# Optimization experiments

Measured on AMD Instinct MI355X. Metric: run time of the kernel, lower is better.

The kernel has to match this reference:

```python
import math
import jax, jax.numpy as jnp
import numpy as np

B, LQ, LK, D, DV = 16, 2048, 2048, 256, 256


def setup_inputs() -> dict:
    key = jax.random.key(0)
    k1, k2, k3, k4 = jax.random.split(key, 4)
    query = jax.random.normal(k1, (B, LQ, D), dtype=jnp.float32)
    kmat = jax.random.normal(k2, (B, LK, D), dtype=jnp.float32)
    value = jax.random.normal(k3, (B, LK, DV), dtype=jnp.float32)
    # per-batch valid lengths in [1, LK] (avoid 0 => all -inf row)
    valid_len = jax.random.randint(k4, (B,), 1, LK + 1, dtype=jnp.int64)
    return {"query": query, "key": kmat, "value": value, "valid_len": valid_len}


def reference(query, key, value, valid_len):
    d = query.shape[-1]
    # [B, Lq, Lk] scaled dot-product scores
    scores = jnp.einsum("bqd,bkd->bqk", query, key) / math.sqrt(d)
    # mask positions k >= valid_len[b] (same mask broadcast over all queries,
    # matching the repeat(1, Lq).view(shape) in the original masked_softmax)
    mask = jnp.arange(key.shape[1])[None, None, :] < valid_len[:, None, None]
    scores = jnp.where(mask, scores, -jnp.inf)
    attn = jax.nn.softmax(scores, axis=-1)  # dropout rate is 0.0 => identity
    return jnp.einsum("bqk,bkv->bqv", attn, value)
```

## Files before the change

### kernel.cpp

```cpp
#include <hip/hip_runtime.h>
#include <hip/hip_bf16.h>

#define B_   16
#define LQ_  2048
#define LK_  2048
#define D_   256
#define DV_  256
#define MINF -1.0e30f

typedef __bf16 bf16x8_t __attribute__((ext_vector_type(8)));
typedef short  s16x8    __attribute__((ext_vector_type(8)));
typedef short  s16x4    __attribute__((ext_vector_type(4)));
typedef float  f32x4    __attribute__((ext_vector_type(4)));

__device__ __forceinline__ unsigned short f2bf(float f) {
  unsigned int u = __builtin_bit_cast(unsigned int, f);
  u += 0x7fffu + ((u >> 16) & 1u);
  return (unsigned short)(u >> 16);
}

__device__ __forceinline__ s16x8 pack8(float4 a, float4 b) {
  s16x8 r;
  r[0] = (short)f2bf(a.x); r[1] = (short)f2bf(a.y);
  r[2] = (short)f2bf(a.z); r[3] = (short)f2bf(a.w);
  r[4] = (short)f2bf(b.x); r[5] = (short)f2bf(b.y);
  r[6] = (short)f2bf(b.z); r[7] = (short)f2bf(b.w);
  return r;
}

__device__ __forceinline__ void glds16(const unsigned short* g, unsigned short* l) {
  __builtin_amdgcn_global_load_lds(
      (const __attribute__((address_space(1))) unsigned int*)g,
      (__attribute__((address_space(3))) unsigned int*)l, 16, 0, 0);
}

__global__ __launch_bounds__(256) void prep_k(const float* __restrict__ K,
                                              unsigned short* __restrict__ wsK) {
  int gid = blockIdx.x * 256 + threadIdx.x;
  int gr = gid >> 5;
  int c  = gid & 31;
  const float* src = K + ((size_t)gr << 8) + c * 8;
  float4 a = *(const float4*)(src);
  float4 b = *(const float4*)(src + 4);
  *(s16x8*)(wsK + ((size_t)gr << 8) + ((c ^ (gr & 7)) << 3)) = pack8(a, b);
}

__global__ __launch_bounds__(256) void prep_v(const float* __restrict__ V,
                                              unsigned short* __restrict__ wsV) {
  __shared__ unsigned short t[256 * 72];
  const int tid = threadIdx.x;
  const float* src = V + (size_t)blockIdx.x * 64 * 256;
  #pragma unroll
  for (int i = 0; i < 16; ++i) {
    int idx = i * 256 + tid;
    int k   = idx >> 6;
    int dv0 = (idx & 63) * 4;
    float4 x = *(const float4*)(src + k * 256 + dv0);
    t[(dv0 + 0) * 72 + k] = f2bf(x.x);
    t[(dv0 + 1) * 72 + k] = f2bf(x.y);
    t[(dv0 + 2) * 72 + k] = f2bf(x.z);
    t[(dv0 + 3) * 72 + k] = f2bf(x.w);
  }
  __syncthreads();
  unsigned short* dst = wsV + (size_t)blockIdx.x * 16384;
  #pragma unroll
  for (int i = 0; i < 8; ++i) {
    int idx = i * 256 + tid;
    int dv = idx >> 3;
    int ch = idx & 7;
    s16x8 v = *(const s16x8*)(&t[dv * 72 + ch * 8]);
    *(s16x8*)(dst + dv * 64 + ((ch ^ (dv & 7)) << 3)) = v;
  }
}

__global__ __launch_bounds__(256) void prep_sched(const int* __restrict__ VL,
                                                  int* __restrict__ sched) {
  __shared__ int ord[16];
  if (threadIdx.x == 0) {
    int nk[16], o[16];
    const int wide = (VL[1] == 0);
    for (int i = 0; i < 16; ++i) {
      int v = wide ? VL[2 * i] : VL[i];
      if (v < 1) v = 1;
      if (v > LK_) v = LK_;
      nk[i] = v; o[i] = i;
    }
    for (int i = 1; i < 16; ++i) {
      int key = o[i], kv = nk[key], j = i - 1;
      while (j >= 0 && nk[o[j]] < kv) { o[j + 1] = o[j]; --j; }
      o[j + 1] = key;
    }
    for (int i = 0; i < 16; ++i) ord[i] = o[i];
  }
  __syncthreads();
  for (int s = threadIdx.x; s < 512; s += 256) {
    int w  = s & 255;
    int un = s >> 8;
    int i  = un ? (511 - w) : w;
    int bsel = ord[i >> 5];
    int qt   = i & 31;
    sched[s] = bsel | (qt << 8);
  }
}

__global__ __launch_bounds__(256, 1) void attn_fwd10(
    const float* __restrict__ Q, const unsigned short* __restrict__ wsK,
    const unsigned short* __restrict__ wsV, const int* __restrict__ VL,
    const int* __restrict__ sched, float* __restrict__ O) {
  __shared__ __align__(16) unsigned short lds_all[70144];

  const int tid  = threadIdx.x;
  const int wid  = tid >> 6;
  const int lane = tid & 63;
  const int l15  = lane & 15;
  const int lg   = lane >> 4;
  const int rq   = wid & 1;
  const int kh   = wid >> 1;

  unsigned short* pw = &lds_all[65536 + wid * 1152];

#define STAGE(buf, t) do {                                                    \
    const unsigned short* ks_ = kbw + (size_t)(t) * 16384;                    \
    const unsigned short* vs_ = vbw + (size_t)(t) * 16384;                    \
    _Pragma("unroll")                                                         \
    for (int p = 0; p < 8; ++p) {                                             \
      int cu = p * 256 + wid * 64;                                            \
      glds16(ks_ + (size_t)(cu + lane) * 8, &lds_all[(buf) * 16384 + cu * 8]);\
      glds16(vs_ + (size_t)(cu + lane) * 8,                                   \
             &lds_all[32768 + (buf) * 16384 + cu * 8]);                       \
    }                                                                         \
  } while (0)

  for (int un = 0; un < 2; ++un) {
    const int e  = sched[blockIdx.x + un * 256];
    const int b  = e & 255;
    const int qt = e >> 8;

    int n_k = (VL[1] == 0) ? VL[2 * b] : VL[b];
    if (n_k < 1) n_k = 1;
    if (n_k > LK_) n_k = LK_;
    const int nt = (n_k + 63) >> 6;

    const int qbase = qt * 64 + rq * 32;

    s16x8 qf[2][8];
    #pragma unroll
    for (int qc = 0; qc < 2; ++qc) {
      const float* qp = Q + ((size_t)b * LQ_ + qbase + qc * 16 + l15) * D_ + lg * 8;
      #pragma unroll
      for (int dk = 0; dk < 8; ++dk) {
        float4 a = *(const float4*)(qp + dk * 32);
        float4 c = *(const float4*)(qp + dk * 32 + 4);
        qf[qc][dk] = pack8(a, c);
      }
    }

    f32x4 o[2][16];
    #pragma unroll
    for (int qc = 0; qc < 2; ++qc)
      #pragma unroll
      for (int c = 0; c < 16; ++c) o[qc][c] = (f32x4){0.f, 0.f, 0.f, 0.f};
    float m[2] = {MINF, MINF}, l[2] = {0.f, 0.f};

    const unsigned short* kbw = wsK + (size_t)b * LK_ * D_;
    const unsigned short* vbw = wsV + (size_t)b * LK_ * DV_;

    __syncthreads();
    STAGE(0, 0);

    for (int t = 0; t < nt; ++t) {
      const int cur = t & 1;
      if (t + 1 < nt) {
        STAGE(cur ^ 1, t + 1);
        asm volatile("s_waitcnt vmcnt(16)" ::: "memory");
      } else {
        asm volatile("s_waitcnt vmcnt(0)" ::: "memory");
      }
      __builtin_amdgcn_s_barrier();
      __builtin_amdgcn_sched_barrier(0);

      const unsigned short* kl = &lds_all[cur * 16384];
      f32x4 s[2][2];
      __builtin_amdgcn_s_setprio(1);
      #pragma unroll
      for (int kc = 0; kc < 2; ++kc) {
        int krow = kh * 32 + kc * 16 + l15;
        int sw = (krow & 7) << 3;
        const unsigned short* kbase = kl + krow * 256;
        f32x4 a0 = (f32x4){0.f, 0.f, 0.f, 0.f};
        f32x4 a1 = (f32x4){0.f, 0.f, 0.f, 0.f};
        #pragma unroll
        for (int dk = 0; dk < 8; ++dk) {
          s16x8 kf = *(const s16x8*)(kbase + ((dk * 32 + lg * 8) ^ sw));
          a0 = __builtin_amdgcn_mfma_f32_16x16x32_bf16(
              __builtin_bit_cast(bf16x8_t, kf),
              __builtin_bit_cast(bf16x8_t, qf[0][dk]), a0, 0, 0, 0);
          a1 = __builtin_amdgcn_mfma_f32_16x16x32_bf16(
              __builtin_bit_cast(bf16x8_t, kf),
              __builtin_bit_cast(bf16x8_t, qf[1][dk]), a1, 0, 0, 0);
        }
        s[kc][0] = a0;
        s[kc][1] = a1;
      }
      __builtin_amdgcn_s_setprio(0);

      #pragma unroll
      for (int kc = 0; kc < 2; ++kc) {
        int gk = t * 64 + kh * 32 + kc * 16 + lg * 4;
        #pragma unroll
        for (int qc = 0; qc < 2; ++qc)
          #pragma unroll
          for (int j2 = 0; j2 < 4; ++j2)
            s[kc][qc][j2] = (gk + j2 < n_k) ? s[kc][qc][j2] * 0.0625f : MINF;
      }

      float pml[2];
      #pragma unroll
      for (int qc = 0; qc < 2; ++qc) {
        float v = fmaxf(fmaxf(s[0][qc][0], s[0][qc][1]),
                        fmaxf(s[0][qc][2], s[0][qc][3]));
        v = fmaxf(v, fmaxf(fmaxf(s[1][qc][0], s[1][qc][1]),
                           fmaxf(s[1][qc][2], s[1][qc][3])));
        pml[qc] = v;
      }
      if (__any((pml[0] > m[0] + 8.0f) || (pml[1] > m[1] + 8.0f))) {
        #pragma unroll
        for (int qc = 0; qc < 2; ++qc) {
          float pm = fmaxf(pml[qc], __shfl_xor(pml[qc], 16, 64));
          pm = fmaxf(pm, __shfl_xor(pm, 32, 64));
          float mn = fmaxf(m[qc], pm);
          float sc = __expf(m[qc] - mn);
          m[qc] = mn; l[qc] *= sc;
          #pragma unroll
          for (int c = 0; c < 16; ++c) o[qc][c] = o[qc][c] * sc;
        }
      }
      #pragma unroll
      for (int qc = 0; qc < 2; ++qc) {
        float p[2][4];
        #pragma unroll
        for (int kc = 0; kc < 2; ++kc)
          #pragma unroll
          for (int j2 = 0; j2 < 4; ++j2)
            p[kc][j2] = __expf(s[kc][qc][j2] - m[qc]);
        l[qc] += ((p[0][0] + p[0][1]) + (p[0][2] + p[0][3]))
               + ((p[1][0] + p[1][1]) + (p[1][2] + p[1][3]));
        #pragma unroll
        for (int kc = 0; kc < 2; ++kc) {
          s16x4 w;
          w[0] = (short)f2bf(p[kc][0]); w[1] = (short)f2bf(p[kc][1]);
          w[2] = (short)f2bf(p[kc][2]); w[3] = (short)f2bf(p[kc][3]);
          *(s16x4*)(pw + (qc * 16 + l15) * 36 + kc * 16 + lg * 4) = w;
        }
      }

      s16x8 pb[2];
      #pragma unroll
      for (int qc = 0; qc < 2; ++qc)
        pb[qc] = *(const s16x8*)(pw + (qc * 16 + l15) * 36 + lg * 8);

      const unsigned short* vl_ = &lds_all[32768 + cur * 16384];
      __builtin_amdgcn_s_setprio(1);
      #pragma unroll
      for (int c = 0; c < 16; ++c) {
        int dv = c * 16 + l15;
        s16x8 vf = *(const s16x8*)(vl_ + dv * 64 + (((kh * 4 + lg) ^ (dv & 7)) << 3));
        o[0][c] = __builtin_amdgcn_mfma_f32_16x16x32_bf16(
            __builtin_bit_cast(bf16x8_t, vf),
            __builtin_bit_cast(bf16x8_t, pb[0]), o[0][c], 0, 0, 0);
        o[1][c] = __builtin_amdgcn_mfma_f32_16x16x32_bf16(
            __builtin_bit_cast(bf16x8_t, vf),
            __builtin_bit_cast(bf16x8_t, pb[1]), o[1][c], 0, 0, 0);
      }
      __builtin_amdgcn_s_setprio(0);

      __builtin_amdgcn_sched_barrier(0);
      __builtin_amdgcn_s_barrier();
    }

    #pragma unroll
    for (int qc = 0; qc < 2; ++qc) {
      l[qc] += __shfl_xor(l[qc], 16, 64);
      l[qc] += __shfl_xor(l[qc], 32, 64);
    }

    __syncthreads();
    float* mo = (float*)lds_all + rq * 8448;
    if (kh == 1) {
      #pragma unroll
      for (int qc = 0; qc < 2; ++qc) {
        #pragma unroll
        for (int c = 0; c < 16; ++c)
          *(f32x4*)(mo + (qc * 16 + l15) * 260 + c * 16 + lg * 4) = o[qc][c];
        mo[8320 + qc * 16 + l15] = m[qc];
        mo[8352 + qc * 16 + l15] = l[qc];
      }
    }
    __syncthreads();
    if (kh == 0) {
      #pragma unroll
      for (int qc = 0; qc < 2; ++qc) {
        float mb = mo[8320 + qc * 16 + l15];
        float lb = mo[8352 + qc * 16 + l15];
        float M  = fmaxf(m[qc], mb);
        float sa = __expf(m[qc] - M), sb = __expf(mb - M);
        float invL = 1.0f / (sa * l[qc] + sb * lb);
        float* ob = O + ((size_t)b * LQ_ + qbase + qc * 16 + l15) * DV_;
        #pragma unroll
        for (int c = 0; c < 16; ++c) {
          int dvb = c * 16 + lg * 4;
          f32x4 mr = *(const f32x4*)(mo + (qc * 16 + l15) * 260 + dvb);
          f32x4 r;
          #pragma unroll
          for (int j2 = 0; j2 < 4; ++j2)
            r[j2] = (sa * o[qc][c][j2] + sb * mr[j2]) * invL;
          *(f32x4*)(ob + dvb) = r;
        }
      }
    }
  }
#undef STAGE
}

__global__ __launch_bounds__(256) void attn_fwd(
    const float* __restrict__ Q, const float* __restrict__ K,
    const float* __restrict__ V, const int* __restrict__ VL,
    float* __restrict__ O) {
  __shared__ __align__(16) unsigned short lds_k[64 * D_];
  __shared__ __align__(16) unsigned short lds_v[DV_ * 64];
  __shared__ __align__(16) unsigned short lds_p[4][16 * 64];

  const int tid  = threadIdx.x;
  const int wid  = tid >> 6;
  const int lane = tid & 63;
  const int l15  = lane & 15;
  const int lg   = lane >> 4;
  const int bid = blockIdx.x;
  const int b   = bid >> 5;
  const int qt  = bid & 31;

  int n_k = (VL[1] == 0) ? VL[2 * b] : VL[b];
  if (n_k < 1) n_k = 1;
  if (n_k > LK_) n_k = LK_;

  const int qbase = qt * 64 + wid * 16;
  s16x8 qf[8];
  {
    const float* qp = Q + ((size_t)b * LQ_ + qbase + l15) * D_ + lg * 8;
    #pragma unroll
    for (int dk = 0; dk < 8; ++dk) {
      float4 a = *(const float4*)(qp + dk * 32);
      float4 c = *(const float4*)(qp + dk * 32 + 4);
      qf[dk] = pack8(a, c);
    }
  }
  f32x4 o[16];
  #pragma unroll
  for (int c = 0; c < 16; ++c) o[c] = (f32x4){0.f, 0.f, 0.f, 0.f};
  float m[4]    = {-INFINITY, -INFINITY, -INFINITY, -INFINITY};
  float lsum[4] = {0.f, 0.f, 0.f, 0.f};
  const float* kb = K + (size_t)b * LK_ * D_;
  const float* vb = V + (size_t)b * LK_ * DV_;
  const int nt = (n_k + 63) / 64;

  for (int kt = 0; kt < nt; ++kt) {
    __syncthreads();
    {
      const float* src = kb + (size_t)kt * 64 * D_;
      #pragma unroll
      for (int p = 0; p < 8; ++p) {
        int e = (p * 256 + tid) * 8;
        int r = e >> 8;
        int d = e & 255;
        float4 a = *(const float4*)(src + e);
        float4 c = *(const float4*)(src + e + 4);
        *(s16x8*)(&lds_k[r * 256 + (d ^ ((r & 7) << 3))]) = pack8(a, c);
      }
    }
    {
      const float* src = vb + (size_t)kt * 64 * DV_;
      #pragma unroll
      for (int p = 0; p < 2; ++p) {
        int item = p * 256 + tid;
        int k0  = (item >> 5) * 4;
        int dv0 = (item & 31) * 8;
        float va[4][8];
        #pragma unroll
        for (int r = 0; r < 4; ++r) {
          float4 x = *(const float4*)(src + (k0 + r) * DV_ + dv0);
          float4 y = *(const float4*)(src + (k0 + r) * DV_ + dv0 + 4);
          va[r][0]=x.x; va[r][1]=x.y; va[r][2]=x.z; va[r][3]=x.w;
          va[r][4]=y.x; va[r][5]=y.y; va[r][6]=y.z; va[r][7]=y.w;
        }
        #pragma unroll
        for (int i = 0; i < 8; ++i) {
          int dv = dv0 + i;
          s16x4 w;
          w[0]=(short)f2bf(va[0][i]); w[1]=(short)f2bf(va[1][i]);
          w[2]=(short)f2bf(va[2][i]); w[3]=(short)f2bf(va[3][i]);
          *(s16x4*)(&lds_v[dv * 64 + (k0 ^ ((dv & 7) << 3))]) = w;
        }
      }
    }
    __syncthreads();

    f32x4 s[4];
    #pragma unroll
    for (int kc = 0; kc < 4; ++kc) {
      f32x4 acc = (f32x4){0.f, 0.f, 0.f, 0.f};
      int krow = kc * 16 + l15;
      int sw = (krow & 7) << 3;
      #pragma unroll
      for (int dk = 0; dk < 8; ++dk) {
        s16x8 kf = *(const s16x8*)(&lds_k[krow * 256 + ((dk * 32 + lg * 8) ^ sw)]);
        acc = __builtin_amdgcn_mfma_f32_16x16x32_bf16(
            __builtin_bit_cast(bf16x8_t, qf[dk]),
            __builtin_bit_cast(bf16x8_t, kf), acc, 0, 0, 0);
      }
      s[kc] = acc;
    }
    #pragma unroll
    for (int kc = 0; kc < 4; ++kc) {
      int gk = kt * 64 + kc * 16 + l15;
      #pragma unroll
      for (int j = 0; j < 4; ++j) {
        float v = s[kc][j] * 0.0625f;
        s[kc][j] = (gk < n_k) ? v : -INFINITY;
      }
    }
    float pm[4];
    #pragma unroll
    for (int j = 0; j < 4; ++j)
      pm[j] = fmaxf(fmaxf(s[0][j], s[1][j]), fmaxf(s[2][j], s[3][j]));
    #pragma unroll
    for (int off = 1; off < 16; off <<= 1) {
      #pragma unroll
      for (int j = 0; j < 4; ++j)
        pm[j] = fmaxf(pm[j], __shfl_xor(pm[j], off, 64));
    }
    float sc[4];
    #pragma unroll
    for (int j = 0; j < 4; ++j) {
      float mn = fmaxf(m[j], pm[j]);
      sc[j] = __expf(m[j] - mn);
      m[j] = mn;
    }
    float psum[4] = {0.f, 0.f, 0.f, 0.f};
    #pragma unroll
    for (int kc = 0; kc < 4; ++kc) {
      #pragma unroll
      for (int j = 0; j < 4; ++j) {
        float p = __expf(s[kc][j] - m[j]);
        psum[j] += p;
        int r2 = lg * 4 + j;
        lds_p[wid][r2 * 64 + ((kc * 16 + l15) ^ ((r2 & 7) << 3))] = f2bf(p);
      }
    }
    #pragma unroll
    for (int off = 1; off < 16; off <<= 1) {
      #pragma unroll
      for (int j = 0; j < 4; ++j)
        psum[j] += __shfl_xor(psum[j], off, 64);
    }
    #pragma unroll
    for (int j = 0; j < 4; ++j) lsum[j] = lsum[j] * sc[j] + psum[j];
    #pragma unroll
    for (int c = 0; c < 16; ++c) {
      #pragma unroll
      for (int j = 0; j < 4; ++j) o[c][j] *= sc[j];
    }
    s16x8 pa[2];
    #pragma unroll
    for (int kk = 0; kk < 2; ++kk)
      pa[kk] = *(const s16x8*)(&lds_p[wid][l15 * 64 + ((kk * 32 + lg * 8) ^ ((l15 & 7) << 3))]);
    #pragma unroll
    for (int c = 0; c < 16; ++c) {
      #pragma unroll
      for (int kk = 0; kk < 2; ++kk) {
        int dv = c * 16 + l15;
        s16x8 vf = *(const s16x8*)(&lds_v[dv * 64 + ((kk * 32 + lg * 8) ^ ((dv & 7) << 3))]);
        o[c] = __builtin_amdgcn_mfma_f32_16x16x32_bf16(
            __builtin_bit_cast(bf16x8_t, pa[kk]),
            __builtin_bit_cast(bf16x8_t, vf), o[c], 0, 0, 0);
      }
    }
  }
  float inv[4];
  #pragma unroll
  for (int j = 0; j < 4; ++j) inv[j] = 1.0f / lsum[j];
  float* ob = O + ((size_t)b * LQ_ + qbase) * DV_;
  #pragma unroll
  for (int c = 0; c < 16; ++c) {
    #pragma unroll
    for (int j = 0; j < 4; ++j) {
      int r2 = lg * 4 + j;
      ob[(size_t)r2 * DV_ + c * 16 + l15] = o[c][j] * inv[j];
    }
  }
}

extern "C" void kernel_launch(void* const* d_in, const int* in_sizes, int n_in,
                              void* d_out, int out_size, void* d_ws, size_t ws_size,
                              hipStream_t stream) {
  const float* Q  = (const float*)d_in[0];
  const float* K  = (const float*)d_in[1];
  const float* V  = (const float*)d_in[2];
  const int*   VL = (const int*)d_in[3];
  float* O = (float*)d_out;

  const size_t kv_elems = (size_t)B_ * LK_ * D_;
  const size_t need = kv_elems * 2 * sizeof(unsigned short) + 2048;
  if (ws_size >= need) {
    unsigned short* wsK = (unsigned short*)d_ws;
    unsigned short* wsV = wsK + kv_elems;
    int* sched = (int*)(wsV + kv_elems);
    prep_sched<<<dim3(1), dim3(256), 0, stream>>>(VL, sched);
    prep_k<<<dim3(4096), dim3(256), 0, stream>>>(K, wsK);
    prep_v<<<dim3(512), dim3(256), 0, stream>>>(V, wsV);
    attn_fwd10<<<dim3(256), dim3(256), 0, stream>>>(Q, wsK, wsV, VL, sched, O);
  } else {
    attn_fwd<<<dim3(512), dim3(256), 0, stream>>>(Q, K, V, VL, O);
  }
}
```

Before: 139.9 us.

## Single-buffer LDS to fit two blocks per CU, launch one block per tile

The attention kernel drops double-buffered K/V staging in LDS, roughly halving shared memory so two blocks can be resident per CU (launch bounds 256,2). Each block now handles one query tile instead of looping over two, the grid doubles to 512, and the schedule interleaves long and short batches. Latency hiding now comes from the co-resident block rather than in-block prefetch. The risks are register pressure under the tighter bound, possible spills, and serialised load/compute within each block.

```diff
diff --git a/kernel.cpp b/kernel.cpp
--- a/kernel.cpp
+++ b/kernel.cpp
@@ -94,20 +94,18 @@
   }
   __syncthreads();
   for (int s = threadIdx.x; s < 512; s += 256) {
-    int w  = s & 255;
-    int un = s >> 8;
-    int i  = un ? (511 - w) : w;
-    int bsel = ord[i >> 5];
-    int qt   = i & 31;
+    int di = (s & 1) ? (511 - (s >> 1)) : (s >> 1);
+    int bsel = ord[di >> 5];
+    int qt   = di & 31;
     sched[s] = bsel | (qt << 8);
   }
 }
 
-__global__ __launch_bounds__(256, 1) void attn_fwd10(
+__global__ __launch_bounds__(256, 2) void attn_fwd11(
     const float* __restrict__ Q, const unsigned short* __restrict__ wsK,
     const unsigned short* __restrict__ wsV, const int* __restrict__ VL,
     const int* __restrict__ sched, float* __restrict__ O) {
-  __shared__ __align__(16) unsigned short lds_all[70144];
+  __shared__ __align__(16) unsigned short lds_all[37376];
 
   const int tid  = threadIdx.x;
   const int wid  = tid >> 6;
@@ -117,205 +115,194 @@
   const int rq   = wid & 1;
   const int kh   = wid >> 1;
 
-  unsigned short* pw = &lds_all[65536 + wid * 1152];
-
-#define STAGE(buf, t) do {                                                    \
+  const int e   = sched[blockIdx.x];
+  const int b   = e & 255;
+  const int qt  = e >> 8;
+
+  int n_k = (VL[1] == 0) ? VL[2 * b] : VL[b];
+  if (n_k < 1) n_k = 1;
+  if (n_k > LK_) n_k = LK_;
+  const int nt = (n_k + 63) >> 6;
+
+  const int qbase = qt * 64 + rq * 32;
+
+  s16x8 qf[2][8];
+  #pragma unroll
+  for (int qc = 0; qc < 2; ++qc) {
+    const float* qp = Q + ((size_t)b * LQ_ + qbase + qc * 16 + l15) * D_ + lg * 8;
+    #pragma unroll
+    for (int dk = 0; dk < 8; ++dk) {
+      float4 a = *(const float4*)(qp + dk * 32);
+      float4 c = *(const float4*)(qp + dk * 32 + 4);
+      qf[qc][dk] = pack8(a, c);
+    }
+  }
+
+  f32x4 o[2][16];
+  #pragma unroll
+  for (int qc = 0; qc < 2; ++qc)
+    #pragma unroll
+    for (int c = 0; c < 16; ++c) o[qc][c] = (f32x4){0.f, 0.f, 0.f, 0.f};
+  float m[2] = {MINF, MINF}, l[2] = {0.f, 0.f};
+
+  const unsigned short* kbw = wsK + (size_t)b * LK_ * D_;
+  const unsigned short* vbw = wsV + (size_t)b * LK_ * DV_;
+  unsigned short* pw = &lds_all[32768 + wid * 1152];
+
+#define STAGE(t) do {                                                         \
     const unsigned short* ks_ = kbw + (size_t)(t) * 16384;                    \
     const unsigned short* vs_ = vbw + (size_t)(t) * 16384;                    \
     _Pragma("unroll")                                                         \
     for (int p = 0; p < 8; ++p) {                                             \
       int cu = p * 256 + wid * 64;                                            \
-      glds16(ks_ + (size_t)(cu + lane) * 8, &lds_all[(buf) * 16384 + cu * 8]);\
-      glds16(vs_ + (size_t)(cu + lane) * 8,                                   \
-             &lds_all[32768 + (buf) * 16384 + cu * 8]);                       \
+      glds16(ks_ + (size_t)(cu + lane) * 8, &lds_all[cu * 8]);                \
+      glds16(vs_ + (size_t)(cu + lane) * 8, &lds_all[16384 + cu * 8]);        \
     }                                                                         \
   } while (0)
 
-  for (int un = 0; un < 2; ++un) {
-    const int e  = sched[blockIdx.x + un * 256];
-    const int b  = e & 255;
-    const int qt = e >> 8;
-
-    int n_k = (VL[1] == 0) ? VL[2 * b] : VL[b];
-    if (n_k < 1) n_k = 1;
-    if (n_k > LK_) n_k = LK_;
-    const int nt = (n_k + 63) >> 6;
-
-    const int qbase = qt * 64 + rq * 32;
-
-    s16x8 qf[2][8];
+  STAGE(0);
+
+  for (int t = 0; t < nt; ++t) {
+    asm volatile("s_waitcnt vmcnt(0)" ::: "memory");
+    __builtin_amdgcn_s_barrier();
+    __builtin_amdgcn_sched_barrier(0);
+
+    f32x4 s[2][2];
+    __builtin_amdgcn_s_setprio(1);
+    #pragma unroll
+    for (int kc = 0; kc < 2; ++kc) {
+      int krow = kh * 32 + kc * 16 + l15;
+      int sw = (krow & 7) << 3;
+      const unsigned short* kbase = &lds_all[krow * 256];
+      f32x4 a0 = (f32x4){0.f, 0.f, 0.f, 0.f};
+      f32x4 a1 = (f32x4){0.f, 0.f, 0.f, 0.f};
+      #pragma unroll
+      for (int dk = 0; dk < 8; ++dk) {
+        s16x8 kf = *(const s16x8*)(kbase + ((dk * 32 + lg * 8) ^ sw));
+        a0 = __builtin_amdgcn_mfma_f32_16x16x32_bf16(
+            __builtin_bit_cast(bf16x8_t, kf),
+            __builtin_bit_cast(bf16x8_t, qf[0][dk]), a0, 0, 0, 0);
+        a1 = __builtin_amdgcn_mfma_f32_16x16x32_bf16(
+            __builtin_bit_cast(bf16x8_t, kf),
+            __builtin_bit_cast(bf16x8_t, qf[1][dk]), a1, 0, 0, 0);
+      }
+      s[kc][0] = a0;
+      s[kc][1] = a1;
+    }
+    __builtin_amdgcn_s_setprio(0);
+
+    #pragma unroll
+    for (int kc = 0; kc < 2; ++kc) {
+      int gk = t * 64 + kh * 32 + kc * 16 + lg * 4;
+      #pragma unroll
+      for (int qc = 0; qc < 2; ++qc)
+        #pragma unroll
+        for (int j2 = 0; j2 < 4; ++j2)
+          s[kc][qc][j2] = (gk + j2 < n_k) ? s[kc][qc][j2] * 0.0625f : MINF;
+    }
+
+    float pml[2];
     #pragma unroll
     for (int qc = 0; qc < 2; ++qc) {
-      const float* qp = Q + ((size_t)b * LQ_ + qbase + qc * 16 + l15) * D_ + lg * 8;
-      #pragma unroll
-      for (int dk = 0; dk < 8; ++dk) {
-        float4 a = *(const float4*)(qp + dk * 32);
-        float4 c = *(const float4*)(qp + dk * 32 + 4);
-        qf[qc][dk] = pack8(a, c);
-      }
-    }
-
-    f32x4 o[2][16];
+      float v = fmaxf(fmaxf(s[0][qc][0], s[0][qc][1]),
+                      fmaxf(s[0][qc][2], s[0][qc][3]));
+      v = fmaxf(v, fmaxf(fmaxf(s[1][qc][0], s[1][qc][1]),
+                         fmaxf(s[1][qc][2], s[1][qc][3])));
+      pml[qc] = v;
+    }
+    if (__any((pml[0] > m[0] + 8.0f) || (pml[1] > m[1] + 8.0f))) {
+      #pragma unroll
+      for (int qc = 0; qc < 2; ++qc) {
+        float pm = fmaxf(pml[qc], __shfl_xor(pml[qc], 16, 64));
+        pm = fmaxf(pm, __shfl_xor(pm, 32, 64));
+        float mn = fmaxf(m[qc], pm);
+        float sc = __expf(m[qc] - mn);
+        m[qc] = mn; l[qc] *= sc;
+        #pragma unroll
+        for (int c = 0; c < 16; ++c) o[qc][c] = o[qc][c] * sc;
+      }
+    }
+    #pragma unroll
+    for (int qc = 0; qc < 2; ++qc) {
+      float p[2][4];
+      #pragma unroll
+      for (int kc = 0; kc < 2; ++kc)
+        #pragma unroll
+        for (int j2 = 0; j2 < 4; ++j2)
+          p[kc][j2] = __expf(s[kc][qc][j2] - m[qc]);
+      l[qc] += ((p[0][0] + p[0][1]) + (p[0][2] + p[0][3]))
+             + ((p[1][0] + p[1][1]) + (p[1][2] + p[1][3]));
+      #pragma unroll
+      for (int kc = 0; kc < 2; ++kc) {
+        s16x4 w;
+        w[0] = (short)f2bf(p[kc][0]); w[1] = (short)f2bf(p[kc][1]);
+        w[2] = (short)f2bf(p[kc][2]); w[3] = (short)f2bf(p[kc][3]);
+        *(s16x4*)(pw + (qc * 16 + l15) * 36 + kc * 16 + lg * 4) = w;
+      }
+    }
+
+    s16x8 pb[2];
     #pragma unroll
     for (int qc = 0; qc < 2; ++qc)
-      #pragma unroll
-      for (int c = 0; c < 16; ++c) o[qc][c] = (f32x4){0.f, 0.f, 0.f, 0.f};
-    float m[2] = {MINF, MINF}, l[2] = {0.f, 0.f};
-
-    const unsigned short* kbw = wsK + (size_t)b * LK_ * D_;
-    const unsigned short* vbw = wsV + (size_t)b * LK_ * DV_;
-
-    __syncthreads();
-    STAGE(0, 0);
-
-    for (int t = 0; t < nt; ++t) {
-      const int cur = t & 1;
-      if (t + 1 < nt) {
-        STAGE(cur ^ 1, t + 1);
-        asm volatile("s_waitcnt vmcnt(16)" ::: "memory");
-      } else {
-        asm volatile("s_waitcnt vmcnt(0)" ::: "memory");
-      }
-      __builtin_amdgcn_s_barrier();
-      __builtin_amdgcn_sched_barrier(0);
-
-      const unsigned short* kl = &lds_all[cur * 16384];
-      f32x4 s[2][2];
-      __builtin_amdgcn_s_setprio(1);
-      #pragma unroll
-      for (int kc = 0; kc < 2; ++kc) {
-        int krow = kh * 32 + kc * 16 + l15;
-        int sw = (krow & 7) << 3;
-        const unsigned short* kbase = kl + krow * 256;
-        f32x4 a0 = (f32x4){0.f, 0.f, 0.f, 0.f};
-        f32x4 a1 = (f32x4){0.f, 0.f, 0.f, 0.f};
+      pb[qc] = *(const s16x8*)(pw + (qc * 16 + l15) * 36 + lg * 8);
+
+    const unsigned short* vl_ = &lds_all[16384];
+    __builtin_amdgcn_s_setprio(1);
+    #pragma unroll
+    for (int c = 0; c < 16; ++c) {
+      int dv = c * 16 + l15;
+      s16x8 vf = *(const s16x8*)(vl_ + dv * 64 + (((kh * 4 + lg) ^ (dv & 7)) << 3));
+      o[0][c] = __builtin_amdgcn_mfma_f32_16x16x32_bf16(
+          __builtin_bit_cast(bf16x8_t, vf),
+          __builtin_bit_cast(bf16x8_t, pb[0]), o[0][c], 0, 0, 0);
+      o[1][c] = __builtin_amdgcn_mfma_f32_16x16x32_bf16(
+          __builtin_bit_cast(bf16x8_t, vf),
+          __builtin_bit_cast(bf16x8_t, pb[1]), o[1][c], 0, 0, 0);
+    }
+    __builtin_amdgcn_s_setprio(0);
+
+    __builtin_amdgcn_sched_barrier(0);
+    __builtin_amdgcn_s_barrier();
+    if (t + 1 < nt) STAGE(t + 1);
+  }
+
+  #pragma unroll
+  for (int qc = 0; qc < 2; ++qc) {
+    l[qc] += __shfl_xor(l[qc], 16, 64);
+    l[qc] += __shfl_xor(l[qc], 32, 64);
+  }
+
+  __syncthreads();
+  float* mo = (float*)lds_all + rq * 8448;
+  if (kh == 1) {
+    #pragma unroll
+    for (int qc = 0; qc < 2; ++qc) {
+      #pragma unroll
+      for (int c = 0; c < 16; ++c)
+        *(f32x4*)(mo + (qc * 16 + l15) * 260 + c * 16 + lg * 4) = o[qc][c];
+      mo[8320 + qc * 16 + l15] = m[qc];
+      mo[8352 + qc * 16 + l15] = l[qc];
+    }
+  }
+  __syncthreads();
+  if (kh == 0) {
+    #pragma unroll
+    for (int qc = 0; qc < 2; ++qc) {
+      float mb = mo[8320 + qc * 16 + l15];
+      float lb = mo[8352 + qc * 16 + l15];
+      float M  = fmaxf(m[qc], mb);
+      float sa = __expf(m[qc] - M), sb = __expf(mb - M);
+      float invL = 1.0f / (sa * l[qc] + sb * lb);
+      float* ob = O + ((size_t)b * LQ_ + qbase + qc * 16 + l15) * DV_;
+      #pragma unroll
+      for (int c = 0; c < 16; ++c) {
+        int dvb = c * 16 + lg * 4;
+        f32x4 mr = *(const f32x4*)(mo + (qc * 16 + l15) * 260 + dvb);
+        f32x4 r;
         #pragma unroll
-        for (int dk = 0; dk < 8; ++dk) {
-          s16x8 kf = *(const s16x8*)(kbase + ((dk * 32 + lg * 8) ^ sw));
-          a0 = __builtin_amdgcn_mfma_f32_16x16x32_bf16(
-              __builtin_bit_cast(bf16x8_t, kf),
-              __builtin_bit_cast(bf16x8_t, qf[0][dk]), a0, 0, 0, 0);
-          a1 = __builtin_amdgcn_mfma_f32_16x16x32_bf16(
-              __builtin_bit_cast(bf16x8_t, kf),
-              __builtin_bit_cast(bf16x8_t, qf[1][dk]), a1, 0, 0, 0);
-        }
-        s[kc][0] = a0;
-        s[kc][1] = a1;
-      }
-      __builtin_amdgcn_s_setprio(0);
-
-      #pragma unroll
-      for (int kc = 0; kc < 2; ++kc) {
-        int gk = t * 64 + kh * 32 + kc * 16 + lg * 4;
-        #pragma unroll
-        for (int qc = 0; qc < 2; ++qc)
-          #pragma unroll
-          for (int j2 = 0; j2 < 4; ++j2)
-            s[kc][qc][j2] = (gk + j2 < n_k) ? s[kc][qc][j2] * 0.0625f : MINF;
-      }
-
-      float pml[2];
-      #pragma unroll
-      for (int qc = 0; qc < 2; ++qc) {
-        float v = fmaxf(fmaxf(s[0][qc][0], s[0][qc][1]),
-                        fmaxf(s[0][qc][2], s[0][qc][3]));
-        v = fmaxf(v, fmaxf(fmaxf(s[1][qc][0], s[1][qc][1]),
-                           fmaxf(s[1][qc][2], s[1][qc][3])));
-        pml[qc] = v;
-      }
-      if (__any((pml[0] > m[0] + 8.0f) || (pml[1] > m[1] + 8.0f))) {
-        #pragma unroll
-        for (int qc = 0; qc < 2; ++qc) {
-          float pm = fmaxf(pml[qc], __shfl_xor(pml[qc], 16, 64));
-          pm = fmaxf(pm, __shfl_xor(pm, 32, 64));
-          float mn = fmaxf(m[qc], pm);
-          float sc = __expf(m[qc] - mn);
-          m[qc] = mn; l[qc] *= sc;
-          #pragma unroll
-          for (int c = 0; c < 16; ++c) o[qc][c] = o[qc][c] * sc;
-        }
-      }
-      #pragma unroll
-      for (int qc = 0; qc < 2; ++qc) {
-        float p[2][4];
-        #pragma unroll
-        for (int kc = 0; kc < 2; ++kc)
-          #pragma unroll
-          for (int j2 = 0; j2 < 4; ++j2)
-            p[kc][j2] = __expf(s[kc][qc][j2] - m[qc]);
-        l[qc] += ((p[0][0] + p[0][1]) + (p[0][2] + p[0][3]))
-               + ((p[1][0] + p[1][1]) + (p[1][2] + p[1][3]));
-        #pragma unroll
-        for (int kc = 0; kc < 2; ++kc) {
-          s16x4 w;
-          w[0] = (short)f2bf(p[kc][0]); w[1] = (short)f2bf(p[kc][1]);
-          w[2] = (short)f2bf(p[kc][2]); w[3] = (short)f2bf(p[kc][3]);
-          *(s16x4*)(pw + (qc * 16 + l15) * 36 + kc * 16 + lg * 4) = w;
-        }
-      }
-
-      s16x8 pb[2];
-      #pragma unroll
-      for (int qc = 0; qc < 2; ++qc)
-        pb[qc] = *(const s16x8*)(pw + (qc * 16 + l15) * 36 + lg * 8);
-
-      const unsigned short* vl_ = &lds_all[32768 + cur * 16384];
-      __builtin_amdgcn_s_setprio(1);
-      #pragma unroll
-      for (int c = 0; c < 16; ++c) {
-        int dv = c * 16 + l15;
-        s16x8 vf = *(const s16x8*)(vl_ + dv * 64 + (((kh * 4 + lg) ^ (dv & 7)) << 3));
-        o[0][c] = __builtin_amdgcn_mfma_f32_16x16x32_bf16(
-            __builtin_bit_cast(bf16x8_t, vf),
-            __builtin_bit_cast(bf16x8_t, pb[0]), o[0][c], 0, 0, 0);
-        o[1][c] = __builtin_amdgcn_mfma_f32_16x16x32_bf16(
-            __builtin_bit_cast(bf16x8_t, vf),
-            __builtin_bit_cast(bf16x8_t, pb[1]), o[1][c], 0, 0, 0);
-      }
-      __builtin_amdgcn_s_setprio(0);
-
-      __builtin_amdgcn_sched_barrier(0);
-      __builtin_amdgcn_s_barrier();
-    }
-
-    #pragma unroll
-    for (int qc = 0; qc < 2; ++qc) {
-      l[qc] += __shfl_xor(l[qc], 16, 64);
-      l[qc] += __shfl_xor(l[qc], 32, 64);
-    }
-
-    __syncthreads();
-    float* mo = (float*)lds_all + rq * 8448;
-    if (kh == 1) {
-      #pragma unroll
-      for (int qc = 0; qc < 2; ++qc) {
-        #pragma unroll
-        for (int c = 0; c < 16; ++c)
-          *(f32x4*)(mo + (qc * 16 + l15) * 260 + c * 16 + lg * 4) = o[qc][c];
-        mo[8320 + qc * 16 + l15] = m[qc];
-        mo[8352 + qc * 16 + l15] = l[qc];
-      }
-    }
-    __syncthreads();
-    if (kh == 0) {
-      #pragma unroll
-      for (int qc = 0; qc < 2; ++qc) {
-        float mb = mo[8320 + qc * 16 + l15];
-        float lb = mo[8352 + qc * 16 + l15];
-        float M  = fmaxf(m[qc], mb);
-        float sa = __expf(m[qc] - M), sb = __expf(mb - M);
-        float invL = 1.0f / (sa * l[qc] + sb * lb);
-        float* ob = O + ((size_t)b * LQ_ + qbase + qc * 16 + l15) * DV_;
-        #pragma unroll
-        for (int c = 0; c < 16; ++c) {
-          int dvb = c * 16 + lg * 4;
-          f32x4 mr = *(const f32x4*)(mo + (qc * 16 + l15) * 260 + dvb);
-          f32x4 r;
-          #pragma unroll
-          for (int j2 = 0; j2 < 4; ++j2)
-            r[j2] = (sa * o[qc][c][j2] + sb * mr[j2]) * invL;
-          *(f32x4*)(ob + dvb) = r;
-        }
+        for (int j2 = 0; j2 < 4; ++j2)
+          r[j2] = (sa * o[qc][c][j2] + sb * mr[j2]) * invL;
+        *(f32x4*)(ob + dvb) = r;
       }
     }
   }
@@ -517,7 +504,7 @@
     prep_sched<<<dim3(1), dim3(256), 0, stream>>>(VL, sched);
     prep_k<<<dim3(4096), dim3(256), 0, stream>>>(K, wsK);
     prep_v<<<dim3(512), dim3(256), 0, stream>>>(V, wsV);
-    attn_fwd10<<<dim3(256), dim3(256), 0, stream>>>(Q, wsK, wsV, VL, sched, O);
+    attn_fwd11<<<dim3(512), dim3(256), 0, stream>>>(Q, wsK, wsV, VL, sched, O);
   } else {
     attn_fwd<<<dim3(512), dim3(256), 0, stream>>>(Q, K, V, VL, O);
   }
```

After: 211.6 us. 51.3% more time.
